# Performance work log

Measured on AMD Instinct MI355X. Metric: run time of the kernel, lower is better.

Reference implementation:

```python
import jax, jax.numpy as jnp
import numpy as np

R_MAX = 5.0          # MACE default cutoff
P_CUT = 6            # polynomial cutoff exponent
AVG_NEIGH = 16.0     # MACE avg_num_neighbors normalization


def _sph_harm(u):
    """Real spherical harmonics l=0..3, e3nn 'component' normalization. u: [E,3] unit vectors -> [E,16]."""
    x, y, z = u[..., 0], u[..., 1], u[..., 2]
    s3, s5, s15 = np.sqrt(3.0), np.sqrt(5.0), np.sqrt(15.0)
    s35_8, s105, s21_8, s7 = np.sqrt(35.0 / 8.0), np.sqrt(105.0), np.sqrt(21.0 / 8.0), np.sqrt(7.0)
    one = jnp.ones_like(x)
    Y = [
        one,
        s3 * x, s3 * y, s3 * z,
        s15 * x * y, s15 * y * z, 0.5 * s5 * (3.0 * z * z - 1.0), s15 * x * z, 0.5 * s15 * (x * x - y * y),
        s35_8 * y * (3.0 * x * x - y * y), s105 * x * y * z, s21_8 * y * (5.0 * z * z - 1.0),
        0.5 * s7 * (5.0 * z * z * z - 3.0 * z), s21_8 * x * (5.0 * z * z - 1.0),
        0.5 * s105 * z * (x * x - y * y), s35_8 * x * (x * x - 3.0 * y * y),
    ]
    return jnp.stack(Y, axis=-1)


def _radial_embedding(r):
    """Bessel basis (8) times polynomial cutoff. r: [E] -> [E,8]."""
    n = jnp.arange(1, 9, dtype=r.dtype)
    rb = np.sqrt(2.0 / R_MAX) * jnp.sin(n * jnp.pi * r[:, None] / R_MAX) / r[:, None]
    uu = jnp.clip(r / R_MAX, 0.0, 1.0)
    p = float(P_CUT)
    f = (1.0 - 0.5 * (p + 1.0) * (p + 2.0) * uu ** p
         + p * (p + 2.0) * uu ** (p + 1.0)
         - 0.5 * p * (p + 1.0) * uu ** (p + 2.0))
    return rb * f[:, None]


def _forward(positions, shifts, node_attrs, W_embed, W_up, W_r1, W_r2, W_lin, W_skip, W_prod, Wcg, Wcg2, edge_index):
    N = positions.shape[0]
    snd, rcv = edge_index[0], edge_index[1]
    vec = positions[rcv] - positions[snd] + shifts            # [E,3]
    r = jnp.sqrt(jnp.maximum(jnp.sum(vec * vec, -1), 1e-12))  # [E]
    u = vec / r[:, None]
    edge_attrs = _sph_harm(u)                                 # [E,16]
    edge_feats = _radial_embedding(r)                         # [E,8]
    L = edge_attrs.shape[-1]
    k = W_embed.shape[1]
    # node embedding: scalars in the l=0 slot
    feats = jnp.zeros((N, k, L), positions.dtype).at[:, :, 0].set(node_attrs @ W_embed)
    invariants = []
    for i in range(W_up.shape[0]):
        up = jnp.einsum('nkL,kc->ncL', feats, W_up[i])                      # linear_up
        Rw = jax.nn.silu(edge_feats @ W_r1[i]) @ W_r2[i]                    # radial MLP [E,k]
        gathered = up[snd] * Rw[:, :, None]                                 # [E,k,16]
        # equivariant tensor product (coupling tensor plays the CG role)
        msg = jnp.einsum('eka,es,ast->ekt', gathered, edge_attrs, Wcg)      # [E,k,16]
        agg = jax.ops.segment_sum(msg, rcv, num_segments=N) / AVG_NEIGH     # scatter-sum
        mid = jnp.einsum('nkL,kc->ncL', agg, W_lin[i])
        # residual skip tensor product with species attrs
        sc = jnp.einsum('nkL,nz,zkc->ncL', feats, node_attrs, W_skip[i])
        # product block: symmetric (quadratic) contraction + linear + skip
        quad = jnp.einsum('nka,nkb,abt->nkt', mid, mid, Wcg2)
        feats = jnp.einsum('nkL,kc->ncL', mid + quad, W_prod[i]) + sc
        invariants.append(feats[:, :, 0])                                   # l=0 invariant slice [N,k]
    return jnp.concatenate(invariants, axis=-1)                             # [N, n_layers*k]


def setup_inputs() -> dict:
    key = jax.random.key(0)
    ks = jax.random.split(key, 12)
    N, E, Z, k, L, NB, H, NL = 8000, 128000, 10, 32, 16, 8, 32, 2
    positions = jax.random.normal(ks[0], (N, 3), dtype=jnp.float32) * 2.0
    edge_index = jax.random.randint(ks[1], (2, E), 0, N, dtype=jnp.int32)
    shifts = jnp.zeros((E, 3), jnp.float32)
    species = jax.random.randint(ks[2], (N,), 0, Z)
    node_attrs = jax.nn.one_hot(species, Z, dtype=jnp.float32)
    W_embed = jax.random.normal(ks[3], (Z, k), dtype=jnp.float32) / np.sqrt(Z)
    W_up = jax.random.normal(ks[4], (NL, k, k), dtype=jnp.float32) / np.sqrt(k)
    W_r1 = jax.random.normal(ks[5], (NL, NB, H), dtype=jnp.float32) / np.sqrt(NB)
    W_r2 = jax.random.normal(ks[6], (NL, H, k), dtype=jnp.float32) / np.sqrt(H)
    W_lin = jax.random.normal(ks[7], (NL, k, k), dtype=jnp.float32) / np.sqrt(k)
    W_skip = jax.random.normal(ks[8], (NL, Z, k, k), dtype=jnp.float32) / np.sqrt(Z * k)
    W_prod = jax.random.normal(ks[9], (NL, k, k), dtype=jnp.float32) / np.sqrt(k)
    Wcg = jax.random.normal(ks[10], (L, L, L), dtype=jnp.float32) * 0.1
    Wcg2 = jax.random.normal(ks[11], (L, L, L), dtype=jnp.float32) * 0.05
    return dict(positions=positions, shifts=shifts, node_attrs=node_attrs, W_embed=W_embed,
                W_up=W_up, W_r1=W_r1, W_r2=W_r2, W_lin=W_lin, W_skip=W_skip, W_prod=W_prod,
                Wcg=Wcg, Wcg2=Wcg2, edge_index=edge_index)


def reference(positions, shifts, node_attrs, W_embed, W_up, W_r1, W_r2, W_lin, W_skip, W_prod, Wcg, Wcg2, edge_index):
    return _forward(positions, shifts, node_attrs, W_embed, W_up, W_r1, W_r2, W_lin, W_skip, W_prod, Wcg, Wcg2, edge_index)
```

## Files before the change

### kernel.cpp

```cpp
#include <hip/hip_runtime.h>
#include <math.h>
#include <stdint.h>

#define N_NODES 8000
#define N_EDGES 128000
#define NZ 10
#define K 32
#define LDIM 16
#define NB 8
#define NH 32
#define NL 2

typedef _Float16 half8 __attribute__((ext_vector_type(8)));
typedef __attribute__((ext_vector_type(4))) float f32x4;

#define WAVE_SYNC() do { \
    asm volatile("s_waitcnt lgkmcnt(0)" ::: "memory"); \
    __builtin_amdgcn_wave_barrier(); \
    __builtin_amdgcn_sched_barrier(0); \
} while (0)

#define NBSTRIDE 640

__global__ __launch_bounds__(256) void k_count(const int* __restrict__ ei,
                                               int* __restrict__ counts) {
    int e = blockIdx.x * 256 + threadIdx.x;
    if (e >= N_EDGES) return;
    atomicAdd(&counts[ei[N_EDGES + e]], 1);
}

__global__ __launch_bounds__(1024) void k_scan(const int* __restrict__ counts,
                                               int* __restrict__ row_ptr,
                                               int* __restrict__ woff) {
    __shared__ int s[8192];
    int tid = threadIdx.x;
    for (int j = tid; j < 8192; j += 1024) s[j] = (j < N_NODES) ? counts[j] : 0;
    __syncthreads();
    for (int off = 1; off < 8192; off <<= 1) {
        int v[8];
#pragma unroll
        for (int jj = 0; jj < 8; jj++) {
            int idx = tid + jj*1024;
            v[jj] = s[idx] + ((idx >= off) ? s[idx - off] : 0);
        }
        __syncthreads();
#pragma unroll
        for (int jj = 0; jj < 8; jj++) s[tid + jj*1024] = v[jj];
        __syncthreads();
    }
    for (int j = tid; j <= N_NODES; j += 1024) {
        int v = (j == 0) ? 0 : s[j-1];
        row_ptr[j] = v;
        if (j < N_NODES) woff[j] = v;
    }
}

__global__ __launch_bounds__(256) void k_scatter(const int* __restrict__ ei,
                                                 int* __restrict__ woff,
                                                 int* __restrict__ inv,
                                                 int* __restrict__ snd_csr) {
    int e = blockIdx.x * 256 + threadIdx.x;
    if (e >= N_EDGES) return;
    int r = ei[N_EDGES + e];
    int s = ei[e];
    int pp = atomicAdd(&woff[r], 1);
    inv[e] = pp;
    snd_csr[pp] = s;
}

__global__ __launch_bounds__(256) void k_geom(const float* __restrict__ pos,
                                              const float* __restrict__ shifts,
                                              const int* __restrict__ ei,
                                              const int* __restrict__ inv,
                                              float* __restrict__ Yc,
                                              float* __restrict__ efc) {
    int e = blockIdx.x * blockDim.x + threadIdx.x;
    if (e >= N_EDGES) return;
    int snd = ei[e];
    int rcv = ei[N_EDGES + e];
    int slot = inv[e];
    float vx = pos[rcv*3+0] - pos[snd*3+0] + shifts[e*3+0];
    float vy = pos[rcv*3+1] - pos[snd*3+1] + shifts[e*3+1];
    float vz = pos[rcv*3+2] - pos[snd*3+2] + shifts[e*3+2];
    float r2 = vx*vx + vy*vy + vz*vz;
    float r  = sqrtf(fmaxf(r2, 1e-12f));
    float inv_r = 1.0f / r;
    float x = vx*inv_r, y = vy*inv_r, z = vz*inv_r;

    const float s3    = 1.7320508075688772f;
    const float s5    = 2.2360679774997896f;
    const float s15   = 3.8729833462074170f;
    const float s35_8 = 2.0916500663351885f;
    const float s105  = 10.246950765959598f;
    const float s21_8 = 1.6201851746019651f;
    const float s7    = 2.6457513110645907f;

    float Yv[16];
    Yv[0]  = 1.0f;
    Yv[1]  = s3*x;  Yv[2] = s3*y;  Yv[3] = s3*z;
    Yv[4]  = s15*x*y;
    Yv[5]  = s15*y*z;
    Yv[6]  = 0.5f*s5*(3.0f*z*z - 1.0f);
    Yv[7]  = s15*x*z;
    Yv[8]  = 0.5f*s15*(x*x - y*y);
    Yv[9]  = s35_8*y*(3.0f*x*x - y*y);
    Yv[10] = s105*x*y*z;
    Yv[11] = s21_8*y*(5.0f*z*z - 1.0f);
    Yv[12] = 0.5f*s7*(5.0f*z*z*z - 3.0f*z);
    Yv[13] = s21_8*x*(5.0f*z*z - 1.0f);
    Yv[14] = 0.5f*s105*z*(x*x - y*y);
    Yv[15] = s35_8*x*(x*x - 3.0f*y*y);
#pragma unroll
    for (int j = 0; j < 16; j++) Yc[(size_t)slot*16 + j] = Yv[j];

    float uu = fminf(fmaxf(r * 0.2f, 0.0f), 1.0f);
    float u2 = uu*uu;
    float u6 = u2*u2*u2;
    float f  = 1.0f - 28.0f*u6 + 48.0f*u6*uu - 21.0f*u6*u2;
    float c  = 0.632455532033676f * inv_r * f;
    const float PI5 = 3.14159265358979323846f * 0.2f;
#pragma unroll
    for (int n = 1; n <= 8; n++) efc[(size_t)slot*8 + n - 1] = c * sinf((float)n * PI5 * r);
}

__global__ __launch_bounds__(256) void k_ww(const float* __restrict__ We,
                                            const float* __restrict__ Wup0,
                                            float* __restrict__ WW) {
    int i = blockIdx.x * 256 + threadIdx.x;
    if (i >= NZ * K) return;
    int z = i >> 5, c = i & 31;
    float a = 0.0f;
#pragma unroll
    for (int k = 0; k < K; ++k) a += We[z*K + k] * Wup0[k*K + c];
    WW[i] = a;
}

__global__ __launch_bounds__(256) void k_wsym(const float* __restrict__ Wcg2,
                                              float* __restrict__ Wsym) {
    int j = blockIdx.x * 256 + threadIdx.x;
    if (j >= 136*16) return;
    int p = j >> 4, t = j & 15;
    int a = 0;
    for (int aa = 1; aa < 16; ++aa)
        if (p >= aa*16 - (aa*(aa-1))/2) a = aa;
    int b = a + (p - (a*16 - (a*(a-1))/2));
    float v = Wcg2[a*256 + b*16 + t];
    if (b > a) v += Wcg2[b*256 + a*16 + t];
    Wsym[j] = v;
}

__global__ __launch_bounds__(256) void k_embed(const float* __restrict__ attrs,
                                               const float* __restrict__ We,
                                               const float* __restrict__ WW,
                                               float* __restrict__ feats,
                                               float* __restrict__ up0c,
                                               int* __restrict__ spec) {
    int i = blockIdx.x * blockDim.x + threadIdx.x;
    if (i >= N_NODES * K) return;
    int n = i >> 5, k = i & 31;
    float a = 0.0f, b = 0.0f;
#pragma unroll
    for (int z = 0; z < NZ; z++) {
        float av = attrs[n*NZ + z];
        a += av * We[z*K + k];
        b += av * WW[z*K + k];
    }
    float* f = feats + (size_t)n*(K*LDIM) + k*LDIM;
    f[0] = a;
#pragma unroll
    for (int j = 1; j < LDIM; j++) f[j] = 0.0f;
    up0c[(size_t)n*K + k] = b;
    if (k == 0) {
        int sp = 0; float best = -1.0f;
        for (int z = 0; z < NZ; z++) { float v = attrs[n*NZ + z]; if (v > best) { best = v; sp = z; } }
        spec[n] = sp;
    }
}

__global__ __launch_bounds__(256) void k_radial(const float* __restrict__ efc,
                                                const float* __restrict__ W1,
                                                const float* __restrict__ W2,
                                                float* __restrict__ Rwc) {
    __shared__ __align__(16) float lW1[NB*NH];
    __shared__ __align__(16) float lW2[NH*K];
    int tid = threadIdx.x;
    for (int j = tid; j < NB*NH; j += 256) lW1[j] = W1[j];
    for (int j = tid; j < NH*K;  j += 256) lW2[j] = W2[j];
    __syncthreads();
    int e = blockIdx.x * 256 + tid;
    if (e >= N_EDGES) return;
    const float4* e4 = (const float4*)(efc + (size_t)e*8);
    float4 ea = e4[0], eb = e4[1];
    float efr[8] = {ea.x, ea.y, ea.z, ea.w, eb.x, eb.y, eb.z, eb.w};
    float rw[32];
#pragma unroll
    for (int k = 0; k < 32; ++k) rw[k] = 0.0f;
    for (int j = 0; j < NH; ++j) {
        float h = 0.0f;
#pragma unroll
        for (int b = 0; b < NB; ++b) h += efr[b] * lW1[b*NH + j];
        float s = h / (1.0f + expf(-h));
        const float4* w2r = (const float4*)(lW2 + j*K);
#pragma unroll
        for (int kq = 0; kq < 8; ++kq) {
            float4 w = w2r[kq];
            rw[kq*4+0] += s*w.x; rw[kq*4+1] += s*w.y;
            rw[kq*4+2] += s*w.z; rw[kq*4+3] += s*w.w;
        }
    }
    float4* o = (float4*)(Rwc + (size_t)e*32);
#pragma unroll
    for (int kq = 0; kq < 8; ++kq)
        o[kq] = make_float4(rw[kq*4], rw[kq*4+1], rw[kq*4+2], rw[kq*4+3]);
}

__device__ __forceinline__ void node_update(float* nb,
                                            const float* lWlin, const float* lWprod,
                                            const float* lWup, const float* lWsym,
                                            const float* __restrict__ Wskip,
                                            float* __restrict__ feats,
                                            const int* __restrict__ spec,
                                            float* __restrict__ out,
                                            int n, int lane, int layer,
                                            _Float16* __restrict__ up_next, int has_up) {
    int c  = lane & 31;
    int th = lane >> 5;
    int to = th * 8;

    float m8[8] = {0,0,0,0,0,0,0,0};
#pragma clang loop unroll_count(4)
    for (int k = 0; k < 32; ++k) {
        float w = lWlin[k*32 + c];
        float4 a0 = *(const float4*)(nb + k*20 + to);
        float4 a1 = *(const float4*)(nb + k*20 + to + 4);
        m8[0]+=a0.x*w; m8[1]+=a0.y*w; m8[2]+=a0.z*w; m8[3]+=a0.w*w;
        m8[4]+=a1.x*w; m8[5]+=a1.y*w; m8[6]+=a1.z*w; m8[7]+=a1.w*w;
    }
    WAVE_SYNC();
    *(float4*)(nb + c*20 + to)     = make_float4(m8[0],m8[1],m8[2],m8[3]);
    *(float4*)(nb + c*20 + to + 4) = make_float4(m8[4],m8[5],m8[6],m8[7]);
    WAVE_SYNC();
    float m[16];
#pragma unroll
    for (int j = 0; j < 4; ++j) {
        float4 v = *(const float4*)(nb + c*20 + j*4);
        m[j*4]=v.x; m[j*4+1]=v.y; m[j*4+2]=v.z; m[j*4+3]=v.w;
    }

    float q8[8] = {0,0,0,0,0,0,0,0};
    {
        int p = 0;
#pragma clang loop unroll(disable)
        for (int a = 0; a < 16; ++a) {
            float ma = m[a];
#pragma clang loop unroll_count(2)
            for (int b = a; b < 16; ++b) {
                float pm = ma * m[b];
                float4 w0 = *(const float4*)(lWsym + p*16 + to);
                float4 w1 = *(const float4*)(lWsym + p*16 + to + 4);
                q8[0]+=pm*w0.x; q8[1]+=pm*w0.y; q8[2]+=pm*w0.z; q8[3]+=pm*w0.w;
                q8[4]+=pm*w1.x; q8[5]+=pm*w1.y; q8[6]+=pm*w1.z; q8[7]+=pm*w1.w;
                ++p;
            }
        }
    }

    WAVE_SYNC();
    *(float4*)(nb + c*20 + to)     = make_float4(m[to]+q8[0],   m[to+1]+q8[1],
                                                 m[to+2]+q8[2], m[to+3]+q8[3]);
    *(float4*)(nb + c*20 + to + 4) = make_float4(m[to+4]+q8[4], m[to+5]+q8[5],
                                                 m[to+6]+q8[6], m[to+7]+q8[7]);
    WAVE_SYNC();

    int sp = spec[n];
    const float* wsk = Wskip + (size_t)sp*1024;
    float* fg = feats + (size_t)n*512;
    float acc8[8] = {0,0,0,0,0,0,0,0};
#pragma clang loop unroll_count(4)
    for (int k = 0; k < 32; ++k) {
        float wp = lWprod[k*32 + c];
        float wv = wsk[k*32 + c];
        float4 s0 = *(const float4*)(nb + k*20 + to);
        float4 s1 = *(const float4*)(nb + k*20 + to + 4);
        float4 f0 = *(const float4*)(fg + k*16 + to);
        float4 f1 = *(const float4*)(fg + k*16 + to + 4);
        acc8[0]+=s0.x*wp+f0.x*wv; acc8[1]+=s0.y*wp+f0.y*wv;
        acc8[2]+=s0.z*wp+f0.z*wv; acc8[3]+=s0.w*wp+f0.w*wv;
        acc8[4]+=s1.x*wp+f1.x*wv; acc8[5]+=s1.y*wp+f1.y*wv;
        acc8[6]+=s1.z*wp+f1.z*wv; acc8[7]+=s1.w*wp+f1.w*wv;
    }
    if (th == 0) out[(size_t)n*(NL*K) + layer*K + c] = acc8[0];
    *(float4*)(fg + c*16 + to)     = make_float4(acc8[0],acc8[1],acc8[2],acc8[3]);
    *(float4*)(fg + c*16 + to + 4) = make_float4(acc8[4],acc8[5],acc8[6],acc8[7]);

    if (has_up) {
        WAVE_SYNC();
        *(float4*)(nb + c*20 + to)     = make_float4(acc8[0],acc8[1],acc8[2],acc8[3]);
        *(float4*)(nb + c*20 + to + 4) = make_float4(acc8[4],acc8[5],acc8[6],acc8[7]);
        WAVE_SYNC();
        float u8[8] = {0,0,0,0,0,0,0,0};
#pragma clang loop unroll_count(4)
        for (int k = 0; k < 32; ++k) {
            float w = lWup[k*32 + c];
            float4 f0 = *(const float4*)(nb + k*20 + to);
            float4 f1 = *(const float4*)(nb + k*20 + to + 4);
            u8[0]+=f0.x*w; u8[1]+=f0.y*w; u8[2]+=f0.z*w; u8[3]+=f0.w*w;
            u8[4]+=f1.x*w; u8[5]+=f1.y*w; u8[6]+=f1.z*w; u8[7]+=f1.w*w;
        }
        half8 h;
#pragma unroll
        for (int j = 0; j < 8; ++j) h[j] = (_Float16)u8[j];
        *(half8*)(up_next + (size_t)n*512 + c*16 + to) = h;
    }
}

__global__ __launch_bounds__(256, 3) void k_fused0(const float* __restrict__ up0c,
                                                   const float* __restrict__ Yc,
                                                   const float* __restrict__ Rwc,
                                                   const int* __restrict__ snd_csr,
                                                   const int* __restrict__ row_ptr,
                                                   const float* __restrict__ Wcg,
                                                   const float* __restrict__ Wlin,
                                                   const float* __restrict__ Wskip,
                                                   const float* __restrict__ Wprod,
                                                   const float* __restrict__ WsymG,
                                                   const float* __restrict__ Wup_next,
                                                   float* __restrict__ feats,
                                                   const int* __restrict__ spec,
                                                   float* __restrict__ out,
                                                   _Float16* __restrict__ up_next) {
    __shared__ __align__(16) float lWlin[1024];
    __shared__ __align__(16) float lWprod[1024];
    __shared__ __align__(16) float lWup[1024];
    __shared__ __align__(16) float lWsym[2176];
    __shared__ __align__(16) float buf[4*NBSTRIDE];

    int tid = threadIdx.x;
    for (int j = tid; j < 1024; j += 256) { lWlin[j] = Wlin[j]; lWprod[j] = Wprod[j]; lWup[j] = Wup_next[j]; }
    for (int j = tid; j < 2176; j += 256) lWsym[j] = WsymG[j];
    __syncthreads();

    int wave = tid >> 6, lane = tid & 63;
    int n = blockIdx.x * 4 + wave;
    int k0 = lane & 15, tq = lane >> 4;
    float* nb = buf + wave*NBSTRIDE;

    float w0[16][4];
#pragma unroll
    for (int s = 0; s < 16; ++s) {
        float4 w = *(const float4*)(Wcg + s*16 + tq*4);
        w0[s][0]=w.x; w0[s][1]=w.y; w0[s][2]=w.z; w0[s][3]=w.w;
    }

    int start = row_ptr[n], end = row_ptr[n+1];
    float4 acc0 = {0,0,0,0}, acc1 = {0,0,0,0};

    if (start < end) {
        int snd = snd_csr[start];
        const float4* Yp = (const float4*)(Yc + (size_t)start*16);
        float4 y0=Yp[0], y1=Yp[1], y2=Yp[2], y3=Yp[3];
        float rw0 = Rwc[(size_t)start*32 + k0];
        float rw1 = Rwc[(size_t)start*32 + 16 + k0];
        float u0 = up0c[(size_t)snd*32 + k0];
        float u1 = up0c[(size_t)snd*32 + 16 + k0];

        for (int ii = start; ii < end; ++ii) {
            int ip = (ii + 1 < end) ? ii + 1 : ii;
            int nsnd = snd_csr[ip];
            const float4* Yn = (const float4*)(Yc + (size_t)ip*16);
            float4 ny0=Yn[0], ny1=Yn[1], ny2=Yn[2], ny3=Yn[3];
            float nrw0 = Rwc[(size_t)ip*32 + k0];
            float nrw1 = Rwc[(size_t)ip*32 + 16 + k0];
            float nu0 = up0c[(size_t)nsnd*32 + k0];
            float nu1 = up0c[(size_t)nsnd*32 + 16 + k0];

            float yv[16] = {y0.x,y0.y,y0.z,y0.w, y1.x,y1.y,y1.z,y1.w,
                            y2.x,y2.y,y2.z,y2.w, y3.x,y3.y,y3.z,y3.w};
            float c0=0.f, c1=0.f, c2=0.f, c3=0.f;
#pragma unroll
            for (int s = 0; s < 16; ++s) {
                c0 += yv[s]*w0[s][0]; c1 += yv[s]*w0[s][1];
                c2 += yv[s]*w0[s][2]; c3 += yv[s]*w0[s][3];
            }
            float g0 = rw0 * u0, g1 = rw1 * u1;
            acc0.x += g0*c0; acc0.y += g0*c1; acc0.z += g0*c2; acc0.w += g0*c3;
            acc1.x += g1*c0; acc1.y += g1*c1; acc1.z += g1*c2; acc1.w += g1*c3;

            y0=ny0; y1=ny1; y2=ny2; y3=ny3;
            rw0=nrw0; rw1=nrw1; u0=nu0; u1=nu1;
        }
    }

    *(float4*)(nb + k0*20 + tq*4)      = make_float4(acc0.x*0.0625f, acc0.y*0.0625f,
                                                     acc0.z*0.0625f, acc0.w*0.0625f);
    *(float4*)(nb + (16+k0)*20 + tq*4) = make_float4(acc1.x*0.0625f, acc1.y*0.0625f,
                                                     acc1.z*0.0625f, acc1.w*0.0625f);
    WAVE_SYNC();

    node_update(nb, lWlin, lWprod, lWup, lWsym, Wskip, feats, spec, out, n, lane, 0, up_next, 1);
}

__global__ __launch_bounds__(256, 2) void k_fused1(const _Float16* __restrict__ up,
                                                   const float* __restrict__ Yc,
                                                   const float* __restrict__ Rwc,
                                                   const int* __restrict__ snd_csr,
                                                   const int* __restrict__ row_ptr,
                                                   const float* __restrict__ Wcg,
                                                   const float* __restrict__ Wlin,
                                                   const float* __restrict__ Wskip,
                                                   const float* __restrict__ Wprod,
                                                   const float* __restrict__ WsymG,
                                                   float* __restrict__ feats,
                                                   const int* __restrict__ spec,
                                                   float* __restrict__ out) {
    __shared__ __align__(16) float lWlin[1024];
    __shared__ __align__(16) float lWprod[1024];
    __shared__ __align__(16) float lWsym[2176];
    __shared__ __align__(16) float buf[4*NBSTRIDE];

    int tid = threadIdx.x;
    for (int j = tid; j < 1024; j += 256) { lWlin[j] = Wlin[j]; lWprod[j] = Wprod[j]; }
    for (int j = tid; j < 2176; j += 256) lWsym[j] = WsymG[j];
    __syncthreads();

    int wave = tid >> 6, lane = tid & 63;
    int n = blockIdx.x * 4 + wave;
    int t0 = lane & 15;
    int g  = lane >> 4;
    int h  = g & 1;
    int eo = g >> 1;
    float* nb = buf + wave*NBSTRIDE;

    float wr[8][16];
#pragma unroll
    for (int j = 0; j < 8; ++j)
#pragma unroll
        for (int s = 0; s < 16; ++s)
            wr[j][s] = Wcg[(8*h + j)*256 + s*16 + t0];

    int start = row_ptr[n], end = row_ptr[n+1];
    f32x4 accL = {0.f,0.f,0.f,0.f}, accH = {0.f,0.f,0.f,0.f};

    if (start < end) {
        int i0 = start + eo;     bool v0 = i0 < end; int q0 = v0 ? i0 : start;
        int i1 = i0 + 2;         bool v1 = i1 < end; int q1 = v1 ? i1 : start;
        int i2 = i0 + 4;         bool v2 = i2 < end; int q2 = v2 ? i2 : start;
        int snd0 = snd_csr[q0], snd1 = snd_csr[q1];
        int snd2 = snd_csr[q2];

        const float4* Y4 = (const float4*)(Yc + (size_t)q0*16);
        float4 y0=Y4[0], y1=Y4[1], y2=Y4[2], y3=Y4[3];
        float rwL = v0 ? Rwc[(size_t)q0*32 + t0]      : 0.0f;
        float rwH = v0 ? Rwc[(size_t)q0*32 + 16 + t0] : 0.0f;
        half8 u0L = *(const half8*)(up + (size_t)snd0*512 + t0*16 + 8*h);
        half8 u0H = *(const half8*)(up + (size_t)snd0*512 + (16+t0)*16 + 8*h);
        half8 u1L = *(const half8*)(up + (size_t)snd1*512 + t0*16 + 8*h);
        half8 u1H = *(const half8*)(up + (size_t)snd1*512 + (16+t0)*16 + 8*h);

        int npair = (end - start + 1) >> 1;
        for (int p = 0; p < npair; ++p) {
            half8 u2L = *(const half8*)(up + (size_t)snd2*512 + t0*16 + 8*h);
            half8 u2H = *(const half8*)(up + (size_t)snd2*512 + (16+t0)*16 + 8*h);
            int in1 = start + 2*(p+1) + eo; bool vn1 = in1 < end; int qn1 = vn1 ? in1 : start;
            const float4* nY = (const float4*)(Yc + (size_t)qn1*16);
            float4 ny0=nY[0], ny1=nY[1], ny2=nY[2], ny3=nY[3];
            float nrwL = vn1 ? Rwc[(size_t)qn1*32 + t0]      : 0.0f;
            float nrwH = vn1 ? Rwc[(size_t)qn1*32 + 16 + t0] : 0.0f;
            int in3 = start + 2*(p+3) + eo; bool vn3 = in3 < end; int qn3 = vn3 ? in3 : start;
            int snd3 = snd_csr[qn3];

            float yv[16] = {y0.x,y0.y,y0.z,y0.w, y1.x,y1.y,y1.z,y1.w,
                            y2.x,y2.y,y2.z,y2.w, y3.x,y3.y,y3.z,y3.w};
            float c[8] = {0,0,0,0,0,0,0,0};
#pragma unroll
            for (int s = 0; s < 16; ++s) {
#pragma unroll
                for (int j = 0; j < 8; ++j) c[j] += yv[s]*wr[j][s];
            }

            half8 bf, rvL, rvH;
            _Float16 rwLh = (_Float16)rwL, rwHh = (_Float16)rwH;
#pragma unroll
            for (int j = 0; j < 8; ++j) { bf[j] = (_Float16)c[j]; rvL[j] = rwLh; rvH[j] = rwHh; }
            half8 afL = u0L * rvL;
            half8 afH = u0H * rvH;

            accL = __builtin_amdgcn_mfma_f32_16x16x32_f16(afL, bf, accL, 0, 0, 0);
            accH = __builtin_amdgcn_mfma_f32_16x16x32_f16(afH, bf, accH, 0, 0, 0);

            y0=ny0; y1=ny1; y2=ny2; y3=ny3;
            rwL=nrwL; rwH=nrwH;
            u0L=u1L; u0H=u1H; u1L=u2L; u1H=u2H;
            snd2 = snd3;
        }
    }

#pragma unroll
    for (int e = 0; e < 4; ++e) {
        nb[(4*g + e)*20 + t0]      = accL[e] * 0.0625f;
        nb[(16 + 4*g + e)*20 + t0] = accH[e] * 0.0625f;
    }
    WAVE_SYNC();

    node_update(nb, lWlin, lWprod, (const float*)nullptr, lWsym, Wskip, feats, spec, out,
                n, lane, 1, (_Float16*)nullptr, 0);
}

extern "C" void kernel_launch(void* const* d_in, const int* in_sizes, int n_in,
                              void* d_out, int out_size, void* d_ws, size_t ws_size,
                              hipStream_t stream) {
    const float* pos     = (const float*)d_in[0];
    const float* shifts  = (const float*)d_in[1];
    const float* attrs   = (const float*)d_in[2];
    const float* W_embed = (const float*)d_in[3];
    const float* W_up    = (const float*)d_in[4];
    const float* W_r1    = (const float*)d_in[5];
    const float* W_r2    = (const float*)d_in[6];
    const float* W_lin   = (const float*)d_in[7];
    const float* W_skip  = (const float*)d_in[8];
    const float* W_prod  = (const float*)d_in[9];
    const float* Wcg     = (const float*)d_in[10];
    const float* Wcg2    = (const float*)d_in[11];
    const int*   ei      = (const int*)d_in[12];
    float* out = (float*)d_out;

    uint8_t* p = (uint8_t*)d_ws;
    auto alloc = [&](size_t bytes) -> void* {
        void* r = (void*)p;
        p += (bytes + 255) & ~size_t(255);
        return r;
    };
    float* Yc        = (float*)alloc((size_t)N_EDGES * 16 * sizeof(float));
    float* efc       = (float*)alloc((size_t)N_EDGES * 8  * sizeof(float));
    float* Rwc0      = (float*)alloc((size_t)N_EDGES * K  * sizeof(float));
    float* Rwc1      = (float*)alloc((size_t)N_EDGES * K  * sizeof(float));
    float* feats     = (float*)alloc((size_t)N_NODES * K * LDIM * sizeof(float));
    _Float16* up_h   = (_Float16*)alloc((size_t)N_NODES * K * LDIM * sizeof(_Float16));
    float* up0c      = (float*)alloc((size_t)N_NODES * K * sizeof(float));
    float* WW        = (float*)alloc((size_t)NZ * K * sizeof(float));
    float* Wsym      = (float*)alloc((size_t)136 * 16 * sizeof(float));
    int* counts   = (int*)alloc((size_t)N_NODES * sizeof(int));
    int* woff     = (int*)alloc((size_t)N_NODES * sizeof(int));
    int* row_ptr  = (int*)alloc((size_t)(N_NODES + 1) * sizeof(int));
    int* inv      = (int*)alloc((size_t)N_EDGES * sizeof(int));
    int* snd_csr  = (int*)alloc((size_t)N_EDGES * sizeof(int));
    int* spec     = (int*)alloc((size_t)N_NODES * sizeof(int));

    hipMemsetAsync(counts, 0, N_NODES * sizeof(int), stream);
    k_count<<<(N_EDGES + 255) / 256, 256, 0, stream>>>(ei, counts);
    k_scan<<<1, 1024, 0, stream>>>(counts, row_ptr, woff);
    k_scatter<<<(N_EDGES + 255) / 256, 256, 0, stream>>>(ei, woff, inv, snd_csr);
    k_geom<<<(N_EDGES + 255) / 256, 256, 0, stream>>>(pos, shifts, ei, inv, Yc, efc);
    k_ww<<<2, 256, 0, stream>>>(W_embed, W_up, WW);
    k_wsym<<<(136*16 + 255) / 256, 256, 0, stream>>>(Wcg2, Wsym);
    k_embed<<<(N_NODES * K + 255) / 256, 256, 0, stream>>>(attrs, W_embed, WW, feats, up0c, spec);

    k_radial<<<(N_EDGES + 255) / 256, 256, 0, stream>>>(efc, W_r1, W_r2, Rwc0);
    k_radial<<<(N_EDGES + 255) / 256, 256, 0, stream>>>(efc, W_r1 + (size_t)1*NB*NH,
                                                        W_r2 + (size_t)1*NH*K, Rwc1);

    k_fused0<<<N_NODES/4, 256, 0, stream>>>(up0c, Yc, Rwc0, snd_csr, row_ptr, Wcg,
                                            W_lin, W_skip, W_prod, Wsym,
                                            W_up + (size_t)1*K*K,
                                            feats, spec, out, up_h);

    k_fused1<<<N_NODES/4, 256, 0, stream>>>(up_h, Yc, Rwc1, snd_csr, row_ptr, Wcg,
                                            W_lin + (size_t)1*K*K,
                                            W_skip + (size_t)1*NZ*K*K,
                                            W_prod + (size_t)1*K*K, Wsym,
                                            feats, spec, out);
}
```

Baseline: 264.1 us.

## Pack CG weights as half2 and read symmetric weights from global memory

In the layer-1 fused kernel, the per-lane CG weight table drops from 128 floats to 64 packed half2 registers. The Y·W contraction becomes packed fp16 multiply-adds, and the launch bound is raised from 2 to 3 blocks per CU. Both fused kernels stop staging the symmetric-product weights in LDS and read them directly from global memory (cached), which removes the 2176-float shared array and its load loop. The aim is lower register and LDS pressure for higher occupancy, at the cost of fp16 accumulation error in the contraction and cache-dependent weight reads in node_update.

```diff
diff --git a/kernel.cpp b/kernel.cpp
--- a/kernel.cpp
+++ b/kernel.cpp
@@ -12,6 +12,7 @@
 #define NL 2
 
 typedef _Float16 half8 __attribute__((ext_vector_type(8)));
+typedef _Float16 half2v __attribute__((ext_vector_type(2)));
 typedef __attribute__((ext_vector_type(4))) float f32x4;
 
 #define WAVE_SYNC() do { \
@@ -216,7 +217,7 @@
 
 __device__ __forceinline__ void node_update(float* nb,
                                             const float* lWlin, const float* lWprod,
-                                            const float* lWup, const float* lWsym,
+                                            const float* lWup, const float* __restrict__ wsym,
                                             const float* __restrict__ Wskip,
                                             float* __restrict__ feats,
                                             const int* __restrict__ spec,
@@ -256,8 +257,8 @@
 #pragma clang loop unroll_count(2)
             for (int b = a; b < 16; ++b) {
                 float pm = ma * m[b];
-                float4 w0 = *(const float4*)(lWsym + p*16 + to);
-                float4 w1 = *(const float4*)(lWsym + p*16 + to + 4);
+                float4 w0 = *(const float4*)(wsym + p*16 + to);
+                float4 w1 = *(const float4*)(wsym + p*16 + to + 4);
                 q8[0]+=pm*w0.x; q8[1]+=pm*w0.y; q8[2]+=pm*w0.z; q8[3]+=pm*w0.w;
                 q8[4]+=pm*w1.x; q8[5]+=pm*w1.y; q8[6]+=pm*w1.z; q8[7]+=pm*w1.w;
                 ++p;
@@ -332,12 +333,10 @@
     __shared__ __align__(16) float lWlin[1024];
     __shared__ __align__(16) float lWprod[1024];
     __shared__ __align__(16) float lWup[1024];
-    __shared__ __align__(16) float lWsym[2176];
     __shared__ __align__(16) float buf[4*NBSTRIDE];
 
     int tid = threadIdx.x;
     for (int j = tid; j < 1024; j += 256) { lWlin[j] = Wlin[j]; lWprod[j] = Wprod[j]; lWup[j] = Wup_next[j]; }
-    for (int j = tid; j < 2176; j += 256) lWsym[j] = WsymG[j];
     __syncthreads();
 
     int wave = tid >> 6, lane = tid & 63;
@@ -397,10 +396,10 @@
                                                      acc1.z*0.0625f, acc1.w*0.0625f);
     WAVE_SYNC();
 
-    node_update(nb, lWlin, lWprod, lWup, lWsym, Wskip, feats, spec, out, n, lane, 0, up_next, 1);
-}
-
-__global__ __launch_bounds__(256, 2) void k_fused1(const _Float16* __restrict__ up,
+    node_update(nb, lWlin, lWprod, lWup, WsymG, Wskip, feats, spec, out, n, lane, 0, up_next, 1);
+}
+
+__global__ __launch_bounds__(256, 3) void k_fused1(const _Float16* __restrict__ up,
                                                    const float* __restrict__ Yc,
                                                    const float* __restrict__ Rwc,
                                                    const int* __restrict__ snd_csr,
@@ -415,12 +414,10 @@
                                                    float* __restrict__ out) {
     __shared__ __align__(16) float lWlin[1024];
     __shared__ __align__(16) float lWprod[1024];
-    __shared__ __align__(16) float lWsym[2176];
     __shared__ __align__(16) float buf[4*NBSTRIDE];
 
     int tid = threadIdx.x;
     for (int j = tid; j < 1024; j += 256) { lWlin[j] = Wlin[j]; lWprod[j] = Wprod[j]; }
-    for (int j = tid; j < 2176; j += 256) lWsym[j] = WsymG[j];
     __syncthreads();
 
     int wave = tid >> 6, lane = tid & 63;
@@ -431,12 +428,16 @@
     int eo = g >> 1;
     float* nb = buf + wave*NBSTRIDE;
 
-    float wr[8][16];
-#pragma unroll
-    for (int j = 0; j < 8; ++j)
-#pragma unroll
-        for (int s = 0; s < 16; ++s)
-            wr[j][s] = Wcg[(8*h + j)*256 + s*16 + t0];
+    half2v wrh[16][4];
+#pragma unroll
+    for (int s = 0; s < 16; ++s)
+#pragma unroll
+        for (int q = 0; q < 4; ++q) {
+            half2v w;
+            w[0] = (_Float16)Wcg[(8*h + 2*q    )*256 + s*16 + t0];
+            w[1] = (_Float16)Wcg[(8*h + 2*q + 1)*256 + s*16 + t0];
+            wrh[s][q] = w;
+        }
 
     int start = row_ptr[n], end = row_ptr[n+1];
     f32x4 accL = {0.f,0.f,0.f,0.f}, accH = {0.f,0.f,0.f,0.f};
@@ -471,17 +472,24 @@
 
             float yv[16] = {y0.x,y0.y,y0.z,y0.w, y1.x,y1.y,y1.z,y1.w,
                             y2.x,y2.y,y2.z,y2.w, y3.x,y3.y,y3.z,y3.w};
-            float c[8] = {0,0,0,0,0,0,0,0};
+            half2v ch[4];
+#pragma unroll
+            for (int q = 0; q < 4; ++q) { half2v z; z[0]=(_Float16)0.f; z[1]=(_Float16)0.f; ch[q]=z; }
 #pragma unroll
             for (int s = 0; s < 16; ++s) {
-#pragma unroll
-                for (int j = 0; j < 8; ++j) c[j] += yv[s]*wr[j][s];
+                _Float16 yh = (_Float16)yv[s];
+                half2v yb; yb[0] = yh; yb[1] = yh;
+#pragma unroll
+                for (int q = 0; q < 4; ++q) ch[q] += yb * wrh[s][q];
             }
-
-            half8 bf, rvL, rvH;
+            half8 bf;
+#pragma unroll
+            for (int q = 0; q < 4; ++q) { bf[2*q] = ch[q][0]; bf[2*q+1] = ch[q][1]; }
+
+            half8 rvL, rvH;
             _Float16 rwLh = (_Float16)rwL, rwHh = (_Float16)rwH;
 #pragma unroll
-            for (int j = 0; j < 8; ++j) { bf[j] = (_Float16)c[j]; rvL[j] = rwLh; rvH[j] = rwHh; }
+            for (int j = 0; j < 8; ++j) { rvL[j] = rwLh; rvH[j] = rwHh; }
             half8 afL = u0L * rvL;
             half8 afH = u0H * rvH;
 
@@ -502,7 +510,7 @@
     }
     WAVE_SYNC();
 
-    node_update(nb, lWlin, lWprod, (const float*)nullptr, lWsym, Wskip, feats, spec, out,
+    node_update(nb, lWlin, lWprod, (const float*)nullptr, WsymG, Wskip, feats, spec, out,
                 n, lane, 1, (_Float16*)nullptr, 0);
 }
 
```

Result: slower. 330.2 us (+25.0%).
